# Optimization experiments

Hardware: AMD Instinct MI355X
Metric: run time of the kernel (lower is better)

## Reference

```python
import jax, jax.numpy as jnp
import numpy as np

B, H, E = 1024, 2048, 1024

def _xavier(key, shape):
    # torch xavier_normal_ on [1, out, in]: std = sqrt(2/(fan_in+fan_out)) over last two dims
    fan_out, fan_in = shape[-2], shape[-1]
    std = (2.0 / (fan_in + fan_out)) ** 0.5
    return jax.random.normal(key, shape, jnp.float32) * std

def setup_inputs() -> dict:
    key = jax.random.key(0)
    ks = jax.random.split(key, 17)
    inp = {
        'x': jax.random.normal(ks[0], (B, E, 1), jnp.float32),
        'c': jax.random.normal(ks[1], (B, H, 1), jnp.float32),
        'h': jax.random.normal(ks[2], (B, H, 1), jnp.float32),
        'W_xi': _xavier(ks[3], (1, H, E)), 'W_hi': _xavier(ks[4], (1, H, H)), 'B_i': _xavier(ks[5], (1, H, 1)),
        'W_xg': _xavier(ks[6], (1, H, E)), 'W_hg': _xavier(ks[7], (1, H, H)), 'B_g': _xavier(ks[8], (1, H, 1)),
        'W_xf': _xavier(ks[9], (1, H, E)), 'W_hf': _xavier(ks[10], (1, H, H)), 'B_f': _xavier(ks[11], (1, H, 1)),
        'W_xo': _xavier(ks[12], (1, H, E)), 'W_ho': _xavier(ks[13], (1, H, H)), 'B_o': _xavier(ks[14], (1, H, 1)),
        'W_hy': _xavier(ks[15], (1, E, H)), 'B_y': _xavier(ks[16], (1, E, 1)),
    }
    return inp

def reference(x, c, h, W_xi, W_hi, B_i, W_xg, W_hg, B_g, W_xf, W_hf, B_f, W_xo, W_ho, B_o, W_hy, B_y):
    # jnp.matmul broadcasts the leading batch dim: [1,H,E] @ [B,E,1] -> [B,H,1]
    i = jax.nn.sigmoid(jnp.matmul(W_xi, x) + jnp.matmul(W_hi, h) + B_i)
    g = jnp.tanh(jnp.matmul(W_xg, x) + jnp.matmul(W_hg, h) + B_g)
    f = jax.nn.sigmoid(jnp.matmul(W_xf, x) + jnp.matmul(W_hf, h) + B_f)
    c_new = f * c + i * g
    o = jax.nn.sigmoid(jnp.matmul(W_xo, x) + jnp.matmul(W_ho, h) + B_o)
    h_new = o * c_new  # NOTE: source uses o*c (no tanh), faithful to original
    y = jnp.tanh(jnp.matmul(W_hy, h_new) + B_y)
    return (y, c_new, h_new)
```

## Files before the change

### kernel.cpp

```cpp
#include <hip/hip_runtime.h>

#define B_SZ 1024
#define H_SZ 2048
#define E_SZ 1024

typedef float  f32x4 __attribute__((ext_vector_type(4)));
typedef short  s16x8 __attribute__((ext_vector_type(8)));

__device__ __forceinline__ unsigned short f2bf(float f) {
    unsigned u = __float_as_uint(f);
    u = u + 0x7fffu + ((u >> 16) & 1u);
    return (unsigned short)(u >> 16);
}
__device__ __forceinline__ float bf2f(unsigned short s) {
    return __uint_as_float(((unsigned)s) << 16);
}
__device__ __forceinline__ float sigm(float v) {
    return 1.0f / (1.0f + __expf(-v));
}
__device__ __forceinline__ unsigned cvtpk(float lo, float hi) {
    unsigned r;
    asm("v_cvt_pk_bf16_f32 %0, %1, %2" : "=v"(r) : "v"(lo), "v"(hi));
    return r;
}

__device__ __forceinline__ void gll(const unsigned short* g, unsigned short* l) {
    __builtin_amdgcn_global_load_lds(
        (const __attribute__((address_space(1))) unsigned int*)g,
        (__attribute__((address_space(3))) unsigned int*)l, 16, 0, 0);
}

struct CastArgs {
    const float*    src[2];
    unsigned short* dst[2];
    int             n[2];
};

__global__ __launch_bounds__(256) void cast_kernel(CastArgs a) {
    const int arr = blockIdx.y;
    const int n = a.n[arr];
    const float* __restrict__ s = a.src[arr];
    unsigned short* __restrict__ d = a.dst[arr];
    const int stride = gridDim.x * 256 * 4;
    for (int i = (blockIdx.x * 256 + threadIdx.x) * 4; i < n; i += stride) {
        float4 v = *(const float4*)(s + i);
        ushort4 o;
        o.x = f2bf(v.x); o.y = f2bf(v.y); o.z = f2bf(v.z); o.w = f2bf(v.w);
        *(ushort4*)(d + i) = o;
    }
}

__device__ __forceinline__ void gemm_accum64_bf32(
    const unsigned short* __restrict__ A,
    const float* __restrict__ W,
    int ld, int kLen, int m0, int n0,
    unsigned short* lA, unsigned short* lB,
    f32x4 acc[4][4], int t)
{
    const int lane = t & 63;
    const int w    = t >> 6;
    const int wr   = (w >> 1) << 6;
    const int wc   = (w & 1) << 6;
    const int lr   = lane & 15;
    const int q4   = lane >> 4;

    const int srow = t >> 3;
    const int scol = ((t & 7) ^ (srow & 7)) << 3;
    const unsigned short* gA = A + (size_t)(m0 + srow) * ld + scol;
    const float*          gB = W + (size_t)(n0 + srow) * ld + scol;
    const size_t st32 = (size_t)32 * ld;

    const int cb0 = ((q4    ) ^ (lr & 7)) << 3;
    const int cb1 = ((4 + q4) ^ (lr & 7)) << 3;

    for (int k0 = 0; k0 < kLen; k0 += 64) {
        float4 f[4][2];
#pragma unroll
        for (int p = 0; p < 4; ++p) {
            const float* src = gB + k0 + p * st32;
            f[p][0] = *(const float4*)(src);
            f[p][1] = *(const float4*)(src + 4);
        }
#pragma unroll
        for (int p = 0; p < 4; ++p)
            gll(gA + k0 + p * st32, lA + (t + 256 * p) * 8);
#pragma unroll
        for (int p = 0; p < 4; ++p) {
            uint4 pk;
            pk.x = cvtpk(f[p][0].x, f[p][0].y);
            pk.y = cvtpk(f[p][0].z, f[p][0].w);
            pk.z = cvtpk(f[p][1].x, f[p][1].y);
            pk.w = cvtpk(f[p][1].z, f[p][1].w);
            *(uint4*)(lB + (t + 256 * p) * 8) = pk;
        }
        __syncthreads();

#pragma unroll
        for (int ks = 0; ks < 2; ++ks) {
            const int cb = ks ? cb1 : cb0;
            s16x8 af[4], bfr[4];
#pragma unroll
            for (int i = 0; i < 4; ++i)
                af[i] = *(const s16x8*)(lA + (wr + i * 16 + lr) * 64 + cb);
#pragma unroll
            for (int j = 0; j < 4; ++j)
                bfr[j] = *(const s16x8*)(lB + (wc + j * 16 + lr) * 64 + cb);
#pragma unroll
            for (int i = 0; i < 4; ++i)
#pragma unroll
                for (int j = 0; j < 4; ++j)
                    acc[i][j] = __builtin_amdgcn_mfma_f32_16x16x32_bf16(
                        af[i], bfr[j], acc[i][j], 0, 0, 0);
        }
        __syncthreads();
    }
}

struct GatesArgs {
    const unsigned short *Xb, *Hb;
    const float *Wx[4], *Wh[4], *bias[4];
    unsigned short *Z;
};

__global__ __launch_bounds__(256) void gates_kernel(GatesArgs a) {
    __shared__ unsigned short lA[128 * 64];
    __shared__ unsigned short lB[128 * 64];
    const int t   = threadIdx.x;
    const int b   = blockIdx.x;
    const int xcd = b & 7;
    const int i_  = b >> 3;
    const int nt  = xcd * 8 + (i_ >> 3);
    const int m0  = (i_ & 7) * 128;
    const int q   = nt >> 4;
    const int n0  = (nt & 15) * 128;

    f32x4 acc[4][4] = {};
    gemm_accum64_bf32(a.Xb, a.Wx[q], E_SZ, E_SZ, m0, n0, lA, lB, acc, t);
    gemm_accum64_bf32(a.Hb, a.Wh[q], H_SZ, H_SZ, m0, n0, lA, lB, acc, t);

    const float* bias = a.bias[q];
    const int lane = t & 63, w = t >> 6;
    const int wr = (w >> 1) << 6, wc = (w & 1) << 6;
    const int lr = lane & 15, rq = (lane >> 4) << 2;
    unsigned short* Zq = a.Z + (size_t)q * B_SZ * H_SZ;
#pragma unroll
    for (int i = 0; i < 4; ++i) {
#pragma unroll
        for (int j = 0; j < 4; ++j) {
            const int n = n0 + wc + j * 16 + lr;
            const float bv = bias[n];
#pragma unroll
            for (int r = 0; r < 4; ++r) {
                const int m = m0 + wr + i * 16 + rq + r;
                const float v = acc[i][j][r] + bv;
                const float act = (q == 1) ? tanhf(v) : sigm(v);
                Zq[(size_t)m * H_SZ + n] = f2bf(act);
            }
        }
    }
}

__global__ __launch_bounds__(256) void cell_kernel(
    const unsigned short* __restrict__ Z, const float* __restrict__ c,
    float* __restrict__ c_out, float* __restrict__ h_out,
    unsigned short* __restrict__ HnB)
{
    const size_t BH = (size_t)B_SZ * H_SZ;
    const int idx = (blockIdx.x * 256 + threadIdx.x) * 4;
    ushort4 iu = *(const ushort4*)(Z + idx);
    ushort4 gu = *(const ushort4*)(Z + BH + idx);
    ushort4 fu = *(const ushort4*)(Z + 2 * BH + idx);
    ushort4 ou = *(const ushort4*)(Z + 3 * BH + idx);
    float4 cv = *(const float4*)(c + idx);

    float cn[4], hn[4];
    cn[0] = bf2f(fu.x) * cv.x + bf2f(iu.x) * bf2f(gu.x);
    cn[1] = bf2f(fu.y) * cv.y + bf2f(iu.y) * bf2f(gu.y);
    cn[2] = bf2f(fu.z) * cv.z + bf2f(iu.z) * bf2f(gu.z);
    cn[3] = bf2f(fu.w) * cv.w + bf2f(iu.w) * bf2f(gu.w);
    hn[0] = bf2f(ou.x) * cn[0];
    hn[1] = bf2f(ou.y) * cn[1];
    hn[2] = bf2f(ou.z) * cn[2];
    hn[3] = bf2f(ou.w) * cn[3];

    *(float4*)(c_out + idx) = make_float4(cn[0], cn[1], cn[2], cn[3]);
    *(float4*)(h_out + idx) = make_float4(hn[0], hn[1], hn[2], hn[3]);
    ushort4 hb;
    hb.x = f2bf(hn[0]); hb.y = f2bf(hn[1]); hb.z = f2bf(hn[2]); hb.w = f2bf(hn[3]);
    *(ushort4*)(HnB + idx) = hb;
}

__global__ __launch_bounds__(256) void y_split_kernel(
    const unsigned short* __restrict__ Hn,
    const float* __restrict__ Wy,
    float* __restrict__ part)
{
    __shared__ unsigned short lA[128 * 64];
    __shared__ unsigned short lB[128 * 64];
    const int t   = threadIdx.x;
    const int b   = blockIdx.x;
    const int xcd = b & 7;
    const int i_  = b >> 3;
    const int ns  = xcd * 4 + (i_ >> 3);
    const int m0  = (i_ & 7) * 128;
    const int n0  = (ns >> 2) * 128;
    const int s   = ns & 3;

    f32x4 acc[4][4] = {};
    gemm_accum64_bf32(Hn + s * 512, Wy + s * 512, H_SZ, 512, m0, n0, lA, lB, acc, t);

    const int lane = t & 63, w = t >> 6;
    const int wr = (w >> 1) << 6, wc = (w & 1) << 6;
    const int lr = lane & 15, rq = (lane >> 4) << 2;
    float* P = part + (size_t)s * B_SZ * E_SZ;
#pragma unroll
    for (int i = 0; i < 4; ++i) {
#pragma unroll
        for (int j = 0; j < 4; ++j) {
            const int n = n0 + wc + j * 16 + lr;
#pragma unroll
            for (int r = 0; r < 4; ++r) {
                const int m = m0 + wr + i * 16 + rq + r;
                P[(size_t)m * E_SZ + n] = acc[i][j][r];
            }
        }
    }
}

__global__ __launch_bounds__(256) void y_reduce_kernel(
    const float* __restrict__ part, const float* __restrict__ by,
    float* __restrict__ yout)
{
    const size_t BE = (size_t)B_SZ * E_SZ;
    const int idx = (blockIdx.x * 256 + threadIdx.x) * 4;
    float4 a = *(const float4*)(part + idx);
    float4 b2 = *(const float4*)(part + BE + idx);
    float4 c2 = *(const float4*)(part + 2 * BE + idx);
    float4 d2 = *(const float4*)(part + 3 * BE + idx);
    const int col = idx & (E_SZ - 1);
    float4 bv = *(const float4*)(by + col);
    float4 o;
    o.x = tanhf(a.x + b2.x + c2.x + d2.x + bv.x);
    o.y = tanhf(a.y + b2.y + c2.y + d2.y + bv.y);
    o.z = tanhf(a.z + b2.z + c2.z + d2.z + bv.z);
    o.w = tanhf(a.w + b2.w + c2.w + d2.w + bv.w);
    *(float4*)(yout + idx) = o;
}

extern "C" void kernel_launch(void* const* d_in, const int* in_sizes, int n_in,
                              void* d_out, int out_size, void* d_ws, size_t ws_size,
                              hipStream_t stream) {
    const float* x   = (const float*)d_in[0];
    const float* c   = (const float*)d_in[1];
    const float* h   = (const float*)d_in[2];
    const float* Wxi = (const float*)d_in[3];
    const float* Whi = (const float*)d_in[4];
    const float* Bi  = (const float*)d_in[5];
    const float* Wxg = (const float*)d_in[6];
    const float* Whg = (const float*)d_in[7];
    const float* Bg  = (const float*)d_in[8];
    const float* Wxf = (const float*)d_in[9];
    const float* Whf = (const float*)d_in[10];
    const float* Bf  = (const float*)d_in[11];
    const float* Wxo = (const float*)d_in[12];
    const float* Who = (const float*)d_in[13];
    const float* Bo  = (const float*)d_in[14];
    const float* Why = (const float*)d_in[15];
    const float* By  = (const float*)d_in[16];

    const size_t BE = (size_t)B_SZ * E_SZ, BH = (size_t)B_SZ * H_SZ;

    unsigned short* ws  = (unsigned short*)d_ws;
    unsigned short* Xb  = ws;
    unsigned short* Hb  = Xb + BE;
    unsigned short* Z   = Hb + BH;
    unsigned short* HnB = Z + 4 * BH;

    CastArgs ca;
    ca.src[0] = x; ca.dst[0] = Xb; ca.n[0] = (int)BE;
    ca.src[1] = h; ca.dst[1] = Hb; ca.n[1] = (int)BH;
    hipLaunchKernelGGL(cast_kernel, dim3(512, 2), dim3(256), 0, stream, ca);

    GatesArgs ga;
    ga.Xb = Xb; ga.Hb = Hb;
    ga.Wx[0] = Wxi; ga.Wx[1] = Wxg; ga.Wx[2] = Wxf; ga.Wx[3] = Wxo;
    ga.Wh[0] = Whi; ga.Wh[1] = Whg; ga.Wh[2] = Whf; ga.Wh[3] = Who;
    ga.bias[0] = Bi; ga.bias[1] = Bg; ga.bias[2] = Bf; ga.bias[3] = Bo;
    ga.Z = Z;
    hipLaunchKernelGGL(gates_kernel, dim3(512), dim3(256), 0, stream, ga);

    float* y_out = (float*)d_out;
    float* c_out = y_out + BE;
    float* h_out = c_out + BH;
    hipLaunchKernelGGL(cell_kernel, dim3((unsigned)(BH / 1024)), dim3(256), 0, stream,
                       Z, c, c_out, h_out, HnB);

    float* ypart = (float*)Z;
    hipLaunchKernelGGL(y_split_kernel, dim3(256), dim3(256), 0, stream,
                       HnB, Why, ypart);
    hipLaunchKernelGGL(y_reduce_kernel, dim3((unsigned)(BE / 1024)), dim3(256), 0, stream,
                       ypart, By, y_out);
}
```

Measured before the change: 282.1 us.

## Double the GEMM K-tile to 128 and prefetch next fp32 weights during MFMA

The shared GEMM helper now stages 128-wide K slices in LDS with a 16-way XOR swizzle. The fp32 weight loads for the next slice are issued into registers right after the barrier, so their global latency overlaps the MFMA work on the current slice. This halves the number of barrier-separated iterations. The trade-off is double the LDS per block (64 KB) and many more live registers for the prefetched weights, with launch bounds hinting two blocks per CU, which may cause spills or lower occupancy.

```diff
diff --git a/kernel.cpp b/kernel.cpp
--- a/kernel.cpp
+++ b/kernel.cpp
@@ -50,7 +50,7 @@
     }
 }
 
-__device__ __forceinline__ void gemm_accum64_bf32(
+__device__ __forceinline__ void gemm_bk128(
     const unsigned short* __restrict__ A,
     const float* __restrict__ W,
     int ld, int kLen, int m0, int n0,
@@ -64,47 +64,59 @@
     const int lr   = lane & 15;
     const int q4   = lane >> 4;
 
-    const int srow = t >> 3;
-    const int scol = ((t & 7) ^ (srow & 7)) << 3;
-    const unsigned short* gA = A + (size_t)(m0 + srow) * ld + scol;
-    const float*          gB = W + (size_t)(n0 + srow) * ld + scol;
-    const size_t st32 = (size_t)32 * ld;
-
-    const int cb0 = ((q4    ) ^ (lr & 7)) << 3;
-    const int cb1 = ((4 + q4) ^ (lr & 7)) << 3;
-
-    for (int k0 = 0; k0 < kLen; k0 += 64) {
-        float4 f[4][2];
-#pragma unroll
-        for (int p = 0; p < 4; ++p) {
-            const float* src = gB + k0 + p * st32;
-            f[p][0] = *(const float4*)(src);
-            f[p][1] = *(const float4*)(src + 4);
-        }
-#pragma unroll
-        for (int p = 0; p < 4; ++p)
-            gll(gA + k0 + p * st32, lA + (t + 256 * p) * 8);
-#pragma unroll
-        for (int p = 0; p < 4; ++p) {
+    const int srow = t >> 4;
+    const int sblk = ((t & 15) ^ srow) << 3;
+    const unsigned short* gA = A + (size_t)(m0 + srow) * ld + sblk;
+    const float*          gW = W + (size_t)(n0 + srow) * ld + sblk;
+    const size_t st16 = (size_t)16 * ld;
+
+    f32x4 f0[8], f1[8];
+#pragma unroll
+    for (int p = 0; p < 8; ++p) {
+        const float* s = gW + p * st16;
+        f0[p] = *(const f32x4*)(s);
+        f1[p] = *(const f32x4*)(s + 4);
+    }
+
+    for (int k0 = 0; k0 < kLen; k0 += 128) {
+#pragma unroll
+        for (int p = 0; p < 8; ++p) {
             uint4 pk;
-            pk.x = cvtpk(f[p][0].x, f[p][0].y);
-            pk.y = cvtpk(f[p][0].z, f[p][0].w);
-            pk.z = cvtpk(f[p][1].x, f[p][1].y);
-            pk.w = cvtpk(f[p][1].z, f[p][1].w);
+            pk.x = cvtpk(f0[p].x, f0[p].y);
+            pk.y = cvtpk(f0[p].z, f0[p].w);
+            pk.z = cvtpk(f1[p].x, f1[p].y);
+            pk.w = cvtpk(f1[p].z, f1[p].w);
             *(uint4*)(lB + (t + 256 * p) * 8) = pk;
         }
+#pragma unroll
+        for (int p = 0; p < 8; ++p)
+            gll(gA + k0 + p * st16, lA + (t + 256 * p) * 8);
         __syncthreads();
 
-#pragma unroll
-        for (int ks = 0; ks < 2; ++ks) {
-            const int cb = ks ? cb1 : cb0;
+        if (k0 + 128 < kLen) {
+#pragma unroll
+            for (int p = 0; p < 8; ++p) {
+                const float* s = gW + (k0 + 128) + p * st16;
+                f0[p] = *(const f32x4*)(s);
+                f1[p] = *(const f32x4*)(s + 4);
+            }
+        }
+
+#pragma unroll
+        for (int ks = 0; ks < 4; ++ks) {
             s16x8 af[4], bfr[4];
 #pragma unroll
-            for (int i = 0; i < 4; ++i)
-                af[i] = *(const s16x8*)(lA + (wr + i * 16 + lr) * 64 + cb);
-#pragma unroll
-            for (int j = 0; j < 4; ++j)
-                bfr[j] = *(const s16x8*)(lB + (wc + j * 16 + lr) * 64 + cb);
+            for (int i = 0; i < 4; ++i) {
+                const int ra = wr + i * 16 + lr;
+                af[i] = *(const s16x8*)(lA + ra * 128 +
+                         ((((ks << 2) + q4) ^ (ra & 15)) << 3));
+            }
+#pragma unroll
+            for (int j = 0; j < 4; ++j) {
+                const int rb = wc + j * 16 + lr;
+                bfr[j] = *(const s16x8*)(lB + rb * 128 +
+                          ((((ks << 2) + q4) ^ (rb & 15)) << 3));
+            }
 #pragma unroll
             for (int i = 0; i < 4; ++i)
 #pragma unroll
@@ -122,9 +134,9 @@
     unsigned short *Z;
 };
 
-__global__ __launch_bounds__(256) void gates_kernel(GatesArgs a) {
-    __shared__ unsigned short lA[128 * 64];
-    __shared__ unsigned short lB[128 * 64];
+__global__ __launch_bounds__(256, 2) void gates_kernel(GatesArgs a) {
+    __shared__ unsigned short lA[128 * 128];
+    __shared__ unsigned short lB[128 * 128];
     const int t   = threadIdx.x;
     const int b   = blockIdx.x;
     const int xcd = b & 7;
@@ -135,8 +147,8 @@
     const int n0  = (nt & 15) * 128;
 
     f32x4 acc[4][4] = {};
-    gemm_accum64_bf32(a.Xb, a.Wx[q], E_SZ, E_SZ, m0, n0, lA, lB, acc, t);
-    gemm_accum64_bf32(a.Hb, a.Wh[q], H_SZ, H_SZ, m0, n0, lA, lB, acc, t);
+    gemm_bk128(a.Xb, a.Wx[q], E_SZ, E_SZ, m0, n0, lA, lB, acc, t);
+    gemm_bk128(a.Hb, a.Wh[q], H_SZ, H_SZ, m0, n0, lA, lB, acc, t);
 
     const float* bias = a.bias[q];
     const int lane = t & 63, w = t >> 6;
@@ -190,13 +202,13 @@
     *(ushort4*)(HnB + idx) = hb;
 }
 
-__global__ __launch_bounds__(256) void y_split_kernel(
+__global__ __launch_bounds__(256, 2) void y_split_kernel(
     const unsigned short* __restrict__ Hn,
     const float* __restrict__ Wy,
     float* __restrict__ part)
 {
-    __shared__ unsigned short lA[128 * 64];
-    __shared__ unsigned short lB[128 * 64];
+    __shared__ unsigned short lA[128 * 128];
+    __shared__ unsigned short lB[128 * 128];
     const int t   = threadIdx.x;
     const int b   = blockIdx.x;
     const int xcd = b & 7;
@@ -207,7 +219,7 @@
     const int s   = ns & 3;
 
     f32x4 acc[4][4] = {};
-    gemm_accum64_bf32(Hn + s * 512, Wy + s * 512, H_SZ, 512, m0, n0, lA, lB, acc, t);
+    gemm_bk128(Hn + s * 512, Wy + s * 512, H_SZ, 512, m0, n0, lA, lB, acc, t);
 
     const int lane = t & 63, w = t >> 6;
     const int wr = (w >> 1) << 6, wc = (w & 1) << 6;
```

Result: faster. 274.5 us (-2.7%).
